# Performance work log

Measured on AMD Instinct MI355X. Metric: run time of the kernel, lower is better.

The kernel has to match this reference:

```python
import jax, jax.numpy as jnp
import numpy as np
import math

NDIM = 16
SCALE = math.sqrt(1.0 / NDIM)


def setup_inputs() -> dict:
    key = jax.random.key(0)
    ks = jax.random.split(key, 7)
    L, Bsz, Dm = 4096, 4, 1024
    return {
        "x": jax.random.normal(ks[0], (L, Bsz, Dm), dtype=jnp.float32),
        "log_dt": jax.random.normal(ks[1], (Dm, 1), dtype=jnp.float32),
        "log_A_real": jax.random.normal(ks[2], (Dm, NDIM), dtype=jnp.float32),
        "A_imag": jax.random.normal(ks[3], (Dm, NDIM), dtype=jnp.float32),
        "B": jax.random.normal(ks[4], (Dm, NDIM, 2), dtype=jnp.float32),
        "C": jax.random.normal(ks[5], (Dm, NDIM, 2), dtype=jnp.float32),
        "D_param": jax.random.normal(ks[6], (Dm,), dtype=jnp.float32),
    }


def _compute_kernel(log_dt, log_A_real, A_imag, B, C, length):
    dt = jnp.exp(log_dt)                                  # (D,1)
    A = -jnp.exp(log_A_real) + 1j * A_imag                # (D,N) complex
    dtA = A * dt                                          # (D,N)
    Cc = (B[..., 0] + 1j * B[..., 1]) * (C[..., 0] + 1j * C[..., 1])  # (D,N)
    # bilinear discretization
    p = Cc * dt / (1.0 - dtA / 2)                         # (D,N)
    log_q = jnp.log((1.0 + dtA / 2) / (1.0 - dtA / 2))    # (D,N)
    # Vandermonde: (D,N,L) complex — the kernel-gen bottleneck
    vander = jnp.exp(jnp.arange(length)[None, None, :] * log_q[:, :, None])
    k = jnp.einsum('dnl,dn->dl', vander, p * SCALE).real  # (D,L)
    return k


def reference(x, log_dt, log_A_real, A_imag, B, C, D_param):
    seq_len, bsz, dim = x.shape
    residual = x * D_param                                # (L,B,D)
    xt = jnp.transpose(x, (1, 2, 0))                      # (B,D,L)
    k = _compute_kernel(log_dt, log_A_real, A_imag, B, C, seq_len)
    fft_len = 2 * seq_len
    k_f = jnp.fft.rfft(k.astype(jnp.float32), n=fft_len)  # (D, fft_len//2+1)
    x_f = jnp.fft.rfft(xt.astype(jnp.float32), n=fft_len)  # (B,D, fft_len//2+1)
    out = jnp.fft.irfft(x_f * k_f, n=fft_len)[..., :seq_len]  # (B,D,L)
    out = out.astype(x.dtype)
    return jax.nn.silu(jnp.transpose(out, (2, 0, 1)) + residual)
```

## Files before the change

kernel.cpp:

```cpp
#include <hip/hip_runtime.h>
#include <math.h>

#define L_SEQ  4096
#define BSZ    4
#define DM     1024
#define NS     16
#define NSH    8
#define NV     (NSH / 2)
#define NCHUNK 64
#define CHUNK  (L_SEQ / NCHUNK)
#define LOG2_CHUNK 6
#define GRP    8
#define NG     (NCHUNK / GRP)
#define SCALE  0.25f
#define LBD    (BSZ * DM)

typedef float v2f __attribute__((ext_vector_type(2)));


__global__ void s4d_params(const float* __restrict__ log_dt,
                           const float* __restrict__ log_A_real,
                           const float* __restrict__ A_imag,
                           const float* __restrict__ Bp,
                           const float* __restrict__ Cp,
                           float2* __restrict__ qbuf,
                           float2* __restrict__ pbuf) {
    int t = blockIdx.x * blockDim.x + threadIdx.x;
    if (t >= NS * DM) return;
    int n = t >> 10, d = t & (DM - 1);
    int i = d * NS + n;
    float dt = expf(log_dt[d]);
    float Ar = -expf(log_A_real[i]);
    float Ai = A_imag[i];
    float ar = 0.5f * Ar * dt, ai = 0.5f * Ai * dt;
    float den_r = 1.0f - ar, den_i = -ai;
    float num_r = 1.0f + ar, num_i = ai;
    float inv = 1.0f / (den_r * den_r + den_i * den_i);
    float qr = (num_r * den_r + num_i * den_i) * inv;
    float qi = (num_i * den_r - num_r * den_i) * inv;
    float B0 = Bp[2 * i], B1 = Bp[2 * i + 1];
    float C0 = Cp[2 * i], C1 = Cp[2 * i + 1];
    float ccr = B0 * C0 - B1 * C1;
    float cci = B0 * C1 + B1 * C0;
    float s = dt * inv * SCALE;
    float pr = (ccr * den_r + cci * den_i) * s;
    float pi = (cci * den_r - ccr * den_i) * s;
    qbuf[t] = make_float2(qr, qi);
    pbuf[t] = make_float2(pr, pi);
}

__attribute__((amdgpu_waves_per_eu(6, 8)))
__global__ __launch_bounds__(256)
void s4d_pass1(const float* __restrict__ x,
               const float2* __restrict__ qbuf,
               float2* __restrict__ S) {
    int tid  = blockIdx.x * 256 + threadIdx.x;
    int lane = tid & 63;
    int dlo  = lane & 31;
    int half = lane >> 5;
    int u    = tid >> 6;
    int dhi  = u & 31;
    int bc   = u >> 5;
    int c    = bc & (NCHUNK - 1);
    int d    = dhi * 32 + dlo;
    int b    = bc >> LOG2_CHUNK;
    int nb   = half * NSH;

    v2f Qr[NV], Qi[NV], Hr[NV], Hi[NV];
#pragma unroll
    for (int k = 0; k < NV; ++k) {
        float2 a = qbuf[(nb + 2 * k) * DM + d];
        float2 bq = qbuf[(nb + 2 * k + 1) * DM + d];
        Qr[k] = (v2f){a.x, bq.x};
        Qi[k] = (v2f){a.y, bq.y};
        Hr[k] = (v2f){0.0f, 0.0f};
        Hi[k] = (v2f){0.0f, 0.0f};
    }
    const float* xp = x + (size_t)(c * CHUNK) * LBD + b * DM + d;
    float xa[8], xb[8], xc[8];
#define LOADX(ARR, L0)                                                        \
    { _Pragma("unroll")                                                       \
      for (int j = 0; j < 8; ++j) ARR[j] = xp[(size_t)((L0) + j) * LBD]; }
#define STEP1(XV)                                                             \
    { v2f X = {XV, XV};                                                       \
      _Pragma("unroll")                                                       \
      for (int k = 0; k < NV; ++k) {                                          \
          v2f nr = __builtin_elementwise_fma(Qr[k], Hr[k],                    \
                    __builtin_elementwise_fma(-Qi[k], Hi[k], X));             \
          v2f ni = __builtin_elementwise_fma(Qr[k], Hi[k], Qi[k] * Hr[k]);    \
          Hr[k] = nr; Hi[k] = ni;                                             \
      } }
#define COMP1(ARR)                                                            \
    { _Pragma("unroll")                                                       \
      for (int j = 0; j < 8; ++j) STEP1(ARR[j]) }
    LOADX(xa, 0)  LOADX(xb, 8)
    LOADX(xc, 16) COMP1(xa)
    LOADX(xa, 24) COMP1(xb)
    LOADX(xb, 32) COMP1(xc)
    LOADX(xc, 40) COMP1(xa)
    LOADX(xa, 48) COMP1(xb)
    LOADX(xb, 56) COMP1(xc)
    COMP1(xa)
    COMP1(xb)
#undef COMP1
#undef STEP1
    float2* sp = S + ((size_t)bc * NS + nb) * DM + d;
#pragma unroll
    for (int k = 0; k < NV; ++k) {
        sp[(size_t)(2 * k) * DM]     = make_float2(Hr[k].x, Hi[k].x);
        sp[(size_t)(2 * k + 1) * DM] = make_float2(Hr[k].y, Hi[k].y);
    }
}

__global__ __launch_bounds__(256)
void s4d_pass2a(const float2* __restrict__ qbuf,
                float2* __restrict__ S,
                float2* __restrict__ GT) {
    int tid = blockIdx.x * 256 + threadIdx.x;
    int d = tid & (DM - 1);
    int n = (tid >> 10) & (NS - 1);
    int g = (tid >> 14) & (NG - 1);
    int b = tid >> 17;
    float2 qv = qbuf[n * DM + d];
    float qr = qv.x, qi = qv.y;
#pragma unroll
    for (int i = 0; i < LOG2_CHUNK; ++i) {
        float nr = qr * qr - qi * qi;
        float ni = 2.0f * qr * qi;
        qr = nr; qi = ni;
    }
    size_t base = ((size_t)(b * NCHUNK + g * GRP) * NS + n) * DM + d;
    const size_t cs = (size_t)NS * DM;
    float2 s0 = S[base + 0 * cs], s1 = S[base + 1 * cs],
           s2 = S[base + 2 * cs], s3 = S[base + 3 * cs],
           s4 = S[base + 4 * cs], s5 = S[base + 5 * cs],
           s6 = S[base + 6 * cs], s7 = S[base + 7 * cs];
    float hr = 0.0f, hi = 0.0f;
#define ST2(J, SB)                                                       \
    {                                                                    \
        S[base + (size_t)(J) * cs] = make_float2(hr, hi);                \
        float nr = fmaf(qr, hr, fmaf(-qi, hi, SB.x));                    \
        float ni = fmaf(qr, hi, fmaf(qi, hr, SB.y));                     \
        hr = nr; hi = ni;                                                \
    }
    ST2(0, s0) ST2(1, s1) ST2(2, s2) ST2(3, s3)
    ST2(4, s4) ST2(5, s5) ST2(6, s6) ST2(7, s7)
#undef ST2
    GT[((size_t)(b * NG + g) * NS + n) * DM + d] = make_float2(hr, hi);
}

__global__ __launch_bounds__(256)
void s4d_pass2b(const float2* __restrict__ qbuf,
                float2* __restrict__ GT) {
    int tid = blockIdx.x * 256 + threadIdx.x;
    int d = tid & (DM - 1);
    int n = (tid >> 10) & (NS - 1);
    int b = tid >> 14;
    float2 qv = qbuf[n * DM + d];
    float qr = qv.x, qi = qv.y;
#pragma unroll
    for (int i = 0; i < LOG2_CHUNK + 3; ++i) {
        float nr = qr * qr - qi * qi;
        float ni = 2.0f * qr * qi;
        qr = nr; qi = ni;
    }
    size_t gbase = ((size_t)(b * NG) * NS + n) * DM + d;
    const size_t gs = (size_t)NS * DM;
    float2 t0 = GT[gbase + 0 * gs], t1 = GT[gbase + 1 * gs],
           t2 = GT[gbase + 2 * gs], t3 = GT[gbase + 3 * gs],
           t4 = GT[gbase + 4 * gs], t5 = GT[gbase + 5 * gs],
           t6 = GT[gbase + 6 * gs], t7 = GT[gbase + 7 * gs];
    float hr = 0.0f, hi = 0.0f;
#define STB(J, SB)                                                       \
    {                                                                    \
        GT[gbase + (size_t)(J) * gs] = make_float2(hr, hi);              \
        float nr = fmaf(qr, hr, fmaf(-qi, hi, SB.x));                    \
        float ni = fmaf(qr, hi, fmaf(qi, hr, SB.y));                     \
        hr = nr; hi = ni;                                                \
    }
    STB(0, t0) STB(1, t1) STB(2, t2) STB(3, t3)
    STB(4, t4) STB(5, t5) STB(6, t6) STB(7, t7)
#undef STB
}

__attribute__((amdgpu_waves_per_eu(4, 4)))
__global__ __launch_bounds__(256)
void s4d_pass3(const float* __restrict__ x,
               const float* __restrict__ Dp,
               const float2* __restrict__ qbuf,
               const float2* __restrict__ pbuf,
               const float2* __restrict__ S,
               const float2* __restrict__ GT,
               float* __restrict__ out) {
    int tid  = blockIdx.x * 256 + threadIdx.x;
    int lane = tid & 63;
    int dlo  = lane & 31;
    int half = lane >> 5;
    int u    = tid >> 6;
    int dhi  = u & 31;
    int bc   = u >> 5;
    int c    = bc & (NCHUNK - 1);
    int d    = dhi * 32 + dlo;
    int b    = bc >> LOG2_CHUNK;
    int nb   = half * NSH;
    int g    = c >> 3;
    int jj   = c & 7;

    v2f Qr[NV], Qi[NV], Pr[NV], Pi[NV], Hr[NV], Hi[NV];
#pragma unroll
    for (int k = 0; k < NV; ++k) {
        float2 a0 = qbuf[(nb + 2 * k) * DM + d];
        float2 a1 = qbuf[(nb + 2 * k + 1) * DM + d];
        float2 w0 = pbuf[(nb + 2 * k) * DM + d];
        float2 w1 = pbuf[(nb + 2 * k + 1) * DM + d];
        Qr[k] = (v2f){a0.x, a1.x};
        Qi[k] = (v2f){a0.y, a1.y};
        Pr[k] = (v2f){w0.x, w1.x};
        Pi[k] = (v2f){w0.y, w1.y};
    }
    const float2* sp = S + ((size_t)bc * NS + nb) * DM + d;
    const float2* gp = GT + ((size_t)(b * NG + g) * NS + nb) * DM + d;
#pragma unroll
    for (int k = 0; k < NV; ++k) {
        float2 s0 = sp[(size_t)(2 * k) * DM];
        float2 s1 = sp[(size_t)(2 * k + 1) * DM];
        float2 g0 = gp[(size_t)(2 * k) * DM];
        float2 g1 = gp[(size_t)(2 * k + 1) * DM];
        v2f Gr = (v2f){g0.x, g1.x};
        v2f Gi = (v2f){g0.y, g1.y};
        v2f ar = Qr[k], ai = Qi[k];
#pragma unroll
        for (int i = 0; i < LOG2_CHUNK; ++i) {
            v2f nr = __builtin_elementwise_fma(-ai, ai, ar * ar);
            v2f ni = (ar + ar) * ai;
            ar = nr; ai = ni;
        }
        v2f wr = (v2f){1.0f, 1.0f}, wi = (v2f){0.0f, 0.0f};
        if (jj & 1) {
            v2f tr = __builtin_elementwise_fma(-wi, ai, wr * ar);
            v2f ti = __builtin_elementwise_fma(wi, ar, wr * ai);
            wr = tr; wi = ti;
        }
        { v2f nr = __builtin_elementwise_fma(-ai, ai, ar * ar);
          v2f ni = (ar + ar) * ai; ar = nr; ai = ni; }
        if (jj & 2) {
            v2f tr = __builtin_elementwise_fma(-wi, ai, wr * ar);
            v2f ti = __builtin_elementwise_fma(wi, ar, wr * ai);
            wr = tr; wi = ti;
        }
        { v2f nr = __builtin_elementwise_fma(-ai, ai, ar * ar);
          v2f ni = (ar + ar) * ai; ar = nr; ai = ni; }
        if (jj & 4) {
            v2f tr = __builtin_elementwise_fma(-wi, ai, wr * ar);
            v2f ti = __builtin_elementwise_fma(wi, ar, wr * ai);
            wr = tr; wi = ti;
        }
        v2f sr = (v2f){s0.x, s1.x};
        v2f si = (v2f){s0.y, s1.y};
        Hr[k] = __builtin_elementwise_fma(wr, Gr,
                 __builtin_elementwise_fma(-wi, Gi, sr));
        Hi[k] = __builtin_elementwise_fma(wr, Gi,
                 __builtin_elementwise_fma(wi, Gr, si));
    }
    float dpar = Dp[d];
    const float* xp = x + (size_t)(c * CHUNK) * LBD + b * DM + d;
    float* op = out + (size_t)(c * CHUNK) * LBD + b * DM + d;
    float xa[8], xb[8], xc[8];
#define COMP3(ARR, L0)                                                        \
    { float av[8];                                                            \
      _Pragma("unroll")                                                       \
      for (int j = 0; j < 8; ++j) {                                           \
          v2f X = {ARR[j], ARR[j]};                                           \
          v2f A = {0.0f, 0.0f};                                               \
          _Pragma("unroll")                                                   \
          for (int k = 0; k < NV; ++k) {                                      \
              v2f nr = __builtin_elementwise_fma(Qr[k], Hr[k],                \
                        __builtin_elementwise_fma(-Qi[k], Hi[k], X));         \
              v2f ni = __builtin_elementwise_fma(Qr[k], Hi[k],                \
                                                 Qi[k] * Hr[k]);              \
              Hr[k] = nr; Hi[k] = ni;                                         \
              A = __builtin_elementwise_fma(Pr[k], nr,                        \
                   __builtin_elementwise_fma(-Pi[k], ni, A));                 \
          }                                                                   \
          av[j] = A.x + A.y;                                                  \
      }                                                                       \
      _Pragma("unroll")                                                       \
      for (int j = 0; j < 8; ++j) av[j] += __shfl_xor(av[j], 32, 64);         \
      if (half == 0) {                                                        \
          _Pragma("unroll")                                                   \
          for (int j = 0; j < 8; ++j) {                                       \
              float z = fmaf(ARR[j], dpar, av[j]);                            \
              float sg = __builtin_amdgcn_rcpf(1.0f + __expf(-z));            \
              op[(size_t)((L0) + j) * LBD] = z * sg;                          \
          }                                                                   \
      } }
    LOADX(xa, 0)  LOADX(xb, 8)
    LOADX(xc, 16) COMP3(xa, 0)
    LOADX(xa, 24) COMP3(xb, 8)
    LOADX(xb, 32) COMP3(xc, 16)
    LOADX(xc, 40) COMP3(xa, 24)
    LOADX(xa, 48) COMP3(xb, 32)
    LOADX(xb, 56) COMP3(xc, 40)
    COMP3(xa, 48)
    COMP3(xb, 56)
#undef COMP3
#undef LOADX
}

extern "C" void kernel_launch(void* const* d_in, const int* in_sizes, int n_in,
                              void* d_out, int out_size, void* d_ws, size_t ws_size,
                              hipStream_t stream) {
    const float* x          = (const float*)d_in[0];
    const float* log_dt     = (const float*)d_in[1];
    const float* log_A_real = (const float*)d_in[2];
    const float* A_imag     = (const float*)d_in[3];
    const float* Bp         = (const float*)d_in[4];
    const float* Cp         = (const float*)d_in[5];
    const float* Dp         = (const float*)d_in[6];
    float* out = (float*)d_out;

    float2* qbuf = (float2*)d_ws;
    float2* pbuf = qbuf + NS * DM;
    float2* S    = pbuf + NS * DM;
    float2* GT   = S + (size_t)BSZ * NCHUNK * NS * DM;

    hipLaunchKernelGGL(s4d_params, dim3((NS * DM) / 256), dim3(256), 0, stream,
                       log_dt, log_A_real, A_imag, Bp, Cp, qbuf, pbuf);
    hipLaunchKernelGGL(s4d_pass1, dim3((2 * BSZ * NCHUNK * DM) / 256), dim3(256), 0, stream,
                       x, qbuf, S);
    hipLaunchKernelGGL(s4d_pass2a, dim3((BSZ * NG * NS * DM) / 256), dim3(256), 0, stream,
                       qbuf, S, GT);
    hipLaunchKernelGGL(s4d_pass2b, dim3((BSZ * NS * DM) / 256), dim3(256), 0, stream,
                       qbuf, GT);
    hipLaunchKernelGGL(s4d_pass3, dim3((2 * BSZ * NCHUNK * DM) / 256), dim3(256), 0, stream,
                       x, Dp, qbuf, pbuf, S, GT, out);
}
```

Baseline: 204.7 us.

## Fuse chunk-state scan into pass1 and pass3, removing two scan kernels

```diff
diff --git a/kernel.cpp b/kernel.cpp
--- a/kernel.cpp
+++ b/kernel.cpp
@@ -50,20 +50,22 @@
 }
 
 __attribute__((amdgpu_waves_per_eu(6, 8)))
-__global__ __launch_bounds__(256)
+__global__ __launch_bounds__(512)
 void s4d_pass1(const float* __restrict__ x,
                const float2* __restrict__ qbuf,
-               float2* __restrict__ S) {
-    int tid  = blockIdx.x * 256 + threadIdx.x;
-    int lane = tid & 63;
+               float2* __restrict__ S,
+               float2* __restrict__ GT) {
+    __shared__ float2 ldsF[GRP * NS * 32];
+    int lane = threadIdx.x & 63;
     int dlo  = lane & 31;
     int half = lane >> 5;
-    int u    = tid >> 6;
-    int dhi  = u & 31;
-    int bc   = u >> 5;
-    int c    = bc & (NCHUNK - 1);
+    int w    = threadIdx.x >> 6;
+    int bx   = blockIdx.x;
+    int g    = bx & (NG - 1);
+    int dhi  = (bx >> 3) & 31;
+    int b    = bx >> 8;
     int d    = dhi * 32 + dlo;
-    int b    = bc >> LOG2_CHUNK;
+    int c    = g * GRP + w;
     int nb   = half * NSH;
 
     v2f Qr[NV], Qi[NV], Hr[NV], Hi[NV];
@@ -104,83 +106,46 @@
     COMP1(xb)
 #undef COMP1
 #undef STEP1
-    float2* sp = S + ((size_t)bc * NS + nb) * DM + d;
+#undef LOADX
+    float2* sp = S + ((size_t)(b * NCHUNK + c) * NS + nb) * DM + d;
 #pragma unroll
     for (int k = 0; k < NV; ++k) {
-        sp[(size_t)(2 * k) * DM]     = make_float2(Hr[k].x, Hi[k].x);
-        sp[(size_t)(2 * k + 1) * DM] = make_float2(Hr[k].y, Hi[k].y);
-    }
-}
-
-__global__ __launch_bounds__(256)
-void s4d_pass2a(const float2* __restrict__ qbuf,
-                float2* __restrict__ S,
-                float2* __restrict__ GT) {
-    int tid = blockIdx.x * 256 + threadIdx.x;
-    int d = tid & (DM - 1);
-    int n = (tid >> 10) & (NS - 1);
-    int g = (tid >> 14) & (NG - 1);
-    int b = tid >> 17;
-    float2 qv = qbuf[n * DM + d];
-    float qr = qv.x, qi = qv.y;
-#pragma unroll
-    for (int i = 0; i < LOG2_CHUNK; ++i) {
-        float nr = qr * qr - qi * qi;
-        float ni = 2.0f * qr * qi;
-        qr = nr; qi = ni;
-    }
-    size_t base = ((size_t)(b * NCHUNK + g * GRP) * NS + n) * DM + d;
-    const size_t cs = (size_t)NS * DM;
-    float2 s0 = S[base + 0 * cs], s1 = S[base + 1 * cs],
-           s2 = S[base + 2 * cs], s3 = S[base + 3 * cs],
-           s4 = S[base + 4 * cs], s5 = S[base + 5 * cs],
-           s6 = S[base + 6 * cs], s7 = S[base + 7 * cs];
-    float hr = 0.0f, hi = 0.0f;
-#define ST2(J, SB)                                                       \
-    {                                                                    \
-        S[base + (size_t)(J) * cs] = make_float2(hr, hi);                \
-        float nr = fmaf(qr, hr, fmaf(-qi, hi, SB.x));                    \
-        float ni = fmaf(qr, hi, fmaf(qi, hr, SB.y));                     \
-        hr = nr; hi = ni;                                                \
-    }
-    ST2(0, s0) ST2(1, s1) ST2(2, s2) ST2(3, s3)
-    ST2(4, s4) ST2(5, s5) ST2(6, s6) ST2(7, s7)
-#undef ST2
-    GT[((size_t)(b * NG + g) * NS + n) * DM + d] = make_float2(hr, hi);
-}
-
-__global__ __launch_bounds__(256)
-void s4d_pass2b(const float2* __restrict__ qbuf,
-                float2* __restrict__ GT) {
-    int tid = blockIdx.x * 256 + threadIdx.x;
-    int d = tid & (DM - 1);
-    int n = (tid >> 10) & (NS - 1);
-    int b = tid >> 14;
-    float2 qv = qbuf[n * DM + d];
-    float qr = qv.x, qi = qv.y;
-#pragma unroll
-    for (int i = 0; i < LOG2_CHUNK + 3; ++i) {
-        float nr = qr * qr - qi * qi;
-        float ni = 2.0f * qr * qi;
-        qr = nr; qi = ni;
-    }
-    size_t gbase = ((size_t)(b * NG) * NS + n) * DM + d;
-    const size_t gs = (size_t)NS * DM;
-    float2 t0 = GT[gbase + 0 * gs], t1 = GT[gbase + 1 * gs],
-           t2 = GT[gbase + 2 * gs], t3 = GT[gbase + 3 * gs],
-           t4 = GT[gbase + 4 * gs], t5 = GT[gbase + 5 * gs],
-           t6 = GT[gbase + 6 * gs], t7 = GT[gbase + 7 * gs];
-    float hr = 0.0f, hi = 0.0f;
-#define STB(J, SB)                                                       \
-    {                                                                    \
-        GT[gbase + (size_t)(J) * gs] = make_float2(hr, hi);              \
-        float nr = fmaf(qr, hr, fmaf(-qi, hi, SB.x));                    \
-        float ni = fmaf(qr, hi, fmaf(qi, hr, SB.y));                     \
-        hr = nr; hi = ni;                                                \
-    }
-    STB(0, t0) STB(1, t1) STB(2, t2) STB(3, t3)
-    STB(4, t4) STB(5, t5) STB(6, t6) STB(7, t7)
-#undef STB
+        float2 f0 = make_float2(Hr[k].x, Hi[k].x);
+        float2 f1 = make_float2(Hr[k].y, Hi[k].y);
+        sp[(size_t)(2 * k) * DM]     = f0;
+        sp[(size_t)(2 * k + 1) * DM] = f1;
+        ldsF[(w * NS + nb + 2 * k) * 32 + dlo]     = f0;
+        ldsF[(w * NS + nb + 2 * k + 1) * 32 + dlo] = f1;
+    }
+    __syncthreads();
+    if (w == GRP - 1) {
+#pragma unroll
+        for (int k = 0; k < NV; ++k) {
+            v2f ar = Qr[k], ai = Qi[k];
+#pragma unroll
+            for (int i = 0; i < LOG2_CHUNK; ++i) {
+                v2f nr = __builtin_elementwise_fma(-ai, ai, ar * ar);
+                v2f ni = (ar + ar) * ai;
+                ar = nr; ai = ni;
+            }
+            v2f tr = (v2f){0.0f, 0.0f}, ti = (v2f){0.0f, 0.0f};
+#pragma unroll
+            for (int w2 = 0; w2 < GRP; ++w2) {
+                float2 f0 = ldsF[(w2 * NS + nb + 2 * k) * 32 + dlo];
+                float2 f1 = ldsF[(w2 * NS + nb + 2 * k + 1) * 32 + dlo];
+                v2f Fr = (v2f){f0.x, f1.x};
+                v2f Fi = (v2f){f0.y, f1.y};
+                v2f nr = __builtin_elementwise_fma(ar, tr,
+                          __builtin_elementwise_fma(-ai, ti, Fr));
+                v2f ni = __builtin_elementwise_fma(ar, ti,
+                          __builtin_elementwise_fma(ai, tr, Fi));
+                tr = nr; ti = ni;
+            }
+            float2* gp = GT + ((size_t)(b * NG + g) * NS + nb) * DM + d;
+            gp[(size_t)(2 * k) * DM]     = make_float2(tr.x, ti.x);
+            gp[(size_t)(2 * k + 1) * DM] = make_float2(tr.y, ti.y);
+        }
+    }
 }
 
 __attribute__((amdgpu_waves_per_eu(4, 4)))
@@ -218,16 +183,8 @@
         Pr[k] = (v2f){w0.x, w1.x};
         Pi[k] = (v2f){w0.y, w1.y};
     }
-    const float2* sp = S + ((size_t)bc * NS + nb) * DM + d;
-    const float2* gp = GT + ((size_t)(b * NG + g) * NS + nb) * DM + d;
 #pragma unroll
     for (int k = 0; k < NV; ++k) {
-        float2 s0 = sp[(size_t)(2 * k) * DM];
-        float2 s1 = sp[(size_t)(2 * k + 1) * DM];
-        float2 g0 = gp[(size_t)(2 * k) * DM];
-        float2 g1 = gp[(size_t)(2 * k + 1) * DM];
-        v2f Gr = (v2f){g0.x, g1.x};
-        v2f Gi = (v2f){g0.y, g1.y};
         v2f ar = Qr[k], ai = Qi[k];
 #pragma unroll
         for (int i = 0; i < LOG2_CHUNK; ++i) {
@@ -235,6 +192,7 @@
             v2f ni = (ar + ar) * ai;
             ar = nr; ai = ni;
         }
+        v2f qLr = ar, qLi = ai;
         v2f wr = (v2f){1.0f, 1.0f}, wi = (v2f){0.0f, 0.0f};
         if (jj & 1) {
             v2f tr = __builtin_elementwise_fma(-wi, ai, wr * ar);
@@ -255,17 +213,48 @@
             v2f ti = __builtin_elementwise_fma(wi, ar, wr * ai);
             wr = tr; wi = ti;
         }
-        v2f sr = (v2f){s0.x, s1.x};
-        v2f si = (v2f){s0.y, s1.y};
-        Hr[k] = __builtin_elementwise_fma(wr, Gr,
-                 __builtin_elementwise_fma(-wi, Gi, sr));
-        Hi[k] = __builtin_elementwise_fma(wr, Gi,
-                 __builtin_elementwise_fma(wi, Gr, si));
+        { v2f nr = __builtin_elementwise_fma(-ai, ai, ar * ar);
+          v2f ni = (ar + ar) * ai; ar = nr; ai = ni; }
+        v2f cr = (v2f){0.0f, 0.0f}, ci = (v2f){0.0f, 0.0f};
+        const float2* gp0 = GT + ((size_t)(b * NG) * NS + nb + 2 * k) * DM + d;
+        const float2* gp1 = GT + ((size_t)(b * NG) * NS + nb + 2 * k + 1) * DM + d;
+        for (int g2 = 0; g2 < g; ++g2) {
+            float2 t0 = gp0[(size_t)g2 * NS * DM];
+            float2 t1 = gp1[(size_t)g2 * NS * DM];
+            v2f Tr = (v2f){t0.x, t1.x};
+            v2f Ti = (v2f){t0.y, t1.y};
+            v2f nr = __builtin_elementwise_fma(ar, cr,
+                      __builtin_elementwise_fma(-ai, ci, Tr));
+            v2f ni = __builtin_elementwise_fma(ar, ci,
+                      __builtin_elementwise_fma(ai, cr, Ti));
+            cr = nr; ci = ni;
+        }
+        v2f sr = (v2f){0.0f, 0.0f}, si = (v2f){0.0f, 0.0f};
+        const float2* fp0 = S + ((size_t)(b * NCHUNK + g * GRP) * NS + nb + 2 * k) * DM + d;
+        const float2* fp1 = S + ((size_t)(b * NCHUNK + g * GRP) * NS + nb + 2 * k + 1) * DM + d;
+        for (int j2 = 0; j2 < jj; ++j2) {
+            float2 f0 = fp0[(size_t)j2 * NS * DM];
+            float2 f1 = fp1[(size_t)j2 * NS * DM];
+            v2f Fr = (v2f){f0.x, f1.x};
+            v2f Fi = (v2f){f0.y, f1.y};
+            v2f nr = __builtin_elementwise_fma(qLr, sr,
+                      __builtin_elementwise_fma(-qLi, si, Fr));
+            v2f ni = __builtin_elementwise_fma(qLr, si,
+                      __builtin_elementwise_fma(qLi, sr, Fi));
+            sr = nr; si = ni;
+        }
+        Hr[k] = __builtin_elementwise_fma(wr, cr,
+                 __builtin_elementwise_fma(-wi, ci, sr));
+        Hi[k] = __builtin_elementwise_fma(wr, ci,
+                 __builtin_elementwise_fma(wi, cr, si));
     }
     float dpar = Dp[d];
     const float* xp = x + (size_t)(c * CHUNK) * LBD + b * DM + d;
     float* op = out + (size_t)(c * CHUNK) * LBD + b * DM + d;
     float xa[8], xb[8], xc[8];
+#define LOADX(ARR, L0)                                                        \
+    { _Pragma("unroll")                                                       \
+      for (int j = 0; j < 8; ++j) ARR[j] = xp[(size_t)((L0) + j) * LBD]; }
 #define COMP3(ARR, L0)                                                        \
     { float av[8];                                                            \
       _Pragma("unroll")                                                       \
@@ -326,12 +315,8 @@
 
     hipLaunchKernelGGL(s4d_params, dim3((NS * DM) / 256), dim3(256), 0, stream,
                        log_dt, log_A_real, A_imag, Bp, Cp, qbuf, pbuf);
-    hipLaunchKernelGGL(s4d_pass1, dim3((2 * BSZ * NCHUNK * DM) / 256), dim3(256), 0, stream,
-                       x, qbuf, S);
-    hipLaunchKernelGGL(s4d_pass2a, dim3((BSZ * NG * NS * DM) / 256), dim3(256), 0, stream,
-                       qbuf, S, GT);
-    hipLaunchKernelGGL(s4d_pass2b, dim3((BSZ * NS * DM) / 256), dim3(256), 0, stream,
-                       qbuf, GT);
+    hipLaunchKernelGGL(s4d_pass1, dim3(BSZ * (DM / 32) * NG), dim3(512), 0, stream,
+                       x, qbuf, S, GT);
     hipLaunchKernelGGL(s4d_pass3, dim3((2 * BSZ * NCHUNK * DM) / 256), dim3(256), 0, stream,
                        x, Dp, qbuf, pbuf, S, GT, out);
 }
```

Measured after the change: 219.2 us. 1.07x slower.
